# Performance work log

Hardware: AMD Instinct MI355X
Metric: run time of the kernel (lower is better)

## Reference

```python
import jax, jax.numpy as jnp
import numpy as np

C = 256
K = C // 2  # inter_channels


def setup_inputs() -> dict:
    key = jax.random.key(0)
    ks = jax.random.split(key, 9)
    B, H, W = 8, 64, 64
    x = jax.random.normal(ks[0], (B, C, H, W), dtype=jnp.float32)
    def lin(k, out_c, in_c, scale):
        return jax.random.normal(k, (out_c, in_c), dtype=jnp.float32) * scale
    s_in = 1.0 / np.sqrt(C)
    s_k = 1.0 / np.sqrt(K)
    return {
        "x": x,
        "theta_w": lin(ks[1], K, C, s_in), "theta_b": jnp.zeros((K,), jnp.float32),
        "phi_w":   lin(ks[2], K, C, s_in), "phi_b":   jnp.zeros((K,), jnp.float32),
        "g_w":     lin(ks[3], K, C, s_in), "g_b":     jnp.zeros((K,), jnp.float32),
        "out_w":   lin(ks[4], C, K, s_k),  "out_b":   jnp.zeros((C,), jnp.float32),
    }


def reference(x, theta_w, theta_b, phi_w, phi_b, g_w, g_b, out_w, out_b):
    B, Cc, H, W = x.shape
    N = H * W
    xf = x.reshape(B, Cc, N)  # [B, C, N]
    # 1x1 convs == per-pixel linear projections
    theta = jnp.einsum('bcn,kc->bnk', xf, theta_w) + theta_b            # [B, N, K]
    phi   = jnp.einsum('bcn,kc->bkn', xf, phi_w) + phi_b[:, None]       # [B, K, N]
    g     = jnp.einsum('bcn,kc->bnk', xf, g_w) + g_b                    # [B, N, K]
    attn = jax.nn.softmax(jnp.einsum('bnk,bkm->bnm', theta, phi), axis=-1)  # [B, N, N]
    y = jnp.einsum('bnm,bmk->bnk', attn, g)                             # [B, N, K]
    out = jnp.einsum('bnk,ck->bcn', y, out_w) + out_b[:, None]          # [B, C, N]
    return out.reshape(B, Cc, H, W) + x
```

## Files before the change

kernel.cpp:

```cpp
#include <hip/hip_runtime.h>

typedef __attribute__((ext_vector_type(8))) _Float16 f16x8;
typedef __attribute__((ext_vector_type(2))) _Float16 f16x2;
typedef __attribute__((ext_vector_type(4))) float f32x4;
typedef __attribute__((ext_vector_type(16))) float f32x16;
typedef __attribute__((ext_vector_type(2))) int int2v;
typedef __attribute__((ext_vector_type(4))) int int4v;

#define DEVI __device__ __forceinline__

DEVI unsigned short f2h(float f){
  _Float16 h = (_Float16)f;
  return __builtin_bit_cast(unsigned short, h);
}
DEVI float fexp2(float x){ return __builtin_amdgcn_exp2f(x); }

__global__ __launch_bounds__(256) void k_wconv(
    const float* __restrict__ tw, const float* __restrict__ pw,
    const float* __restrict__ gw, const float* __restrict__ ow,
    unsigned short* __restrict__ dst){
  int i = blockIdx.x*256 + threadIdx.x;
  int a = i>>15, off = i & 32767;
  const float* s = (a==0)?tw:(a==1)?pw:(a==2)?gw:ow;
  dst[i] = f2h(s[off]);
}

__global__ __launch_bounds__(256) void k_proj(
    const float* __restrict__ x,
    const unsigned short* __restrict__ Wq, const unsigned short* __restrict__ Wk,
    const unsigned short* __restrict__ Wg,
    const float* __restrict__ tb, const float* __restrict__ pb,
    const float* __restrict__ gb,
    unsigned short* __restrict__ Q, unsigned short* __restrict__ Km,
    unsigned short* __restrict__ VT)
{
  __shared__ __align__(16) unsigned short xT[64*264];
  const int tid = threadIdx.x;
  const int w = tid>>6, l = tid&63, l15 = l&15, lhi = l>>4;
  const int b = blockIdx.y, n0 = blockIdx.x*64;

  const float* xb = x + (size_t)b*256*4096 + n0;
  #pragma unroll 4
  for (int i=0;i<32;++i){
    int c = 64*w + 2*i;
    float v0 = xb[(size_t)c*4096 + l];
    float v1 = xb[(size_t)(c+1)*4096 + l];
    unsigned int pk = (unsigned int)f2h(v0) | ((unsigned int)f2h(v1)<<16);
    *(unsigned int*)&xT[l*264 + c] = pk;
  }
  __syncthreads();

  for (int mat=0; mat<2; ++mat){
    const unsigned short* Wm = mat ? Wk : Wq;
    const float* bias = mat ? pb : tb;
    unsigned short* Out = mat ? Km : Q;
    const float scl = mat ? 1.0f : 1.44269504f;
    for (int pbk=0; pbk<4; ++pbk){
      f16x8 aF[8];
      #pragma unroll
      for (int ks=0;ks<8;++ks)
        aF[ks] = *(const f16x8*)&xT[(16*pbk + l15)*264 + lhi*8 + 32*ks];
      #pragma unroll
      for (int kb2=0; kb2<2; ++kb2){
        int kb = 2*w + kb2;
        f32x4 acc = {0.f,0.f,0.f,0.f};
        #pragma unroll
        for (int ks=0;ks<8;++ks){
          f16x8 bF = *(const f16x8*)&Wm[(size_t)(16*kb + l15)*256 + lhi*8 + 32*ks];
          acc = __builtin_amdgcn_mfma_f32_16x16x32_f16(aF[ks], bF, acc, 0,0,0);
        }
        float bv = bias[16*kb + l15];
        #pragma unroll
        for (int r=0;r<4;++r){
          int pix = 16*pbk + lhi*4 + r;
          Out[((size_t)b*4096 + n0 + pix)*128 + 16*kb + l15] = f2h((acc[r] + bv)*scl);
        }
      }
    }
  }

  for (int nb=0; nb<4; ++nb){
    f16x8 bF[8];
    #pragma unroll
    for (int ks=0;ks<8;++ks)
      bF[ks] = *(const f16x8*)&xT[(16*nb + l15)*264 + lhi*8 + 32*ks];
    #pragma unroll
    for (int mb2=0; mb2<2; ++mb2){
      int mb = 2*w + mb2;
      f32x4 acc = {0.f,0.f,0.f,0.f};
      #pragma unroll
      for (int ks=0;ks<8;++ks){
        f16x8 aF = *(const f16x8*)&Wg[(size_t)(16*mb + l15)*256 + lhi*8 + 32*ks];
        acc = __builtin_amdgcn_mfma_f32_16x16x32_f16(aF, bF[ks], acc, 0,0,0);
      }
      #pragma unroll
      for (int r=0;r<4;++r){
        int k = 16*mb + lhi*4 + r;
        VT[((size_t)b*128 + k)*4096 + n0 + 16*nb + l15] = f2h(acc[r] + gb[k]);
      }
    }
  }
}

DEVI void stage_tiles(const char* Kg, const char* Vg, int nt,
                      char* Kd, char* Vd, int w, int l){
  #pragma unroll
  for (int c=0;c<4;++c){
    int base = (4*w + c)*1024;
    int lin  = base + l*16;
    int row = lin>>8, colb = lin&255;
    int f = ((row&7) ^ ((row>>2)&4)) << 4;
    const char* g = Kg + (size_t)(nt*64 + row)*256 + (colb ^ f);
    __builtin_amdgcn_global_load_lds((const __attribute__((address_space(1))) void*)g,
        (__attribute__((address_space(3))) void*)(Kd + base), 16, 0, 0);
  }
  #pragma unroll
  for (int c=0;c<4;++c){
    int base = (4*w + c)*1024;
    int lin  = base + l*16;
    int row = lin>>7, colb = lin&127;
    int f = ((row&7) ^ ((row>>2)&4)) << 4;
    const char* g = Vg + (size_t)row*8192 + (size_t)nt*128 + (colb ^ f);
    __builtin_amdgcn_global_load_lds((const __attribute__((address_space(1))) void*)g,
        (__attribute__((address_space(3))) void*)(Vd + base), 16, 0, 0);
  }
}

__global__ __launch_bounds__(256, 2) void k_attn(
    const unsigned short* __restrict__ Q, const unsigned short* __restrict__ Km,
    const unsigned short* __restrict__ VT,
    unsigned short* __restrict__ On,
    float* __restrict__ Mp, float* __restrict__ Lp)
{
  __shared__ __align__(16) unsigned short K_lds[2][64*128];
  __shared__ __align__(16) unsigned short V_lds[2][128*64];
  const int tid = threadIdx.x;
  const int w = tid>>6, l = tid&63;
  const int q32 = l & 31, hi = l >> 5;
  const int qt = blockIdx.x, h = blockIdx.y, b = blockIdx.z;
  const int n0 = qt*128, wq0 = w*32, nt0 = h*32;
  const int swz = ((q32&7) ^ ((q32>>2)&4)) << 4;

  const unsigned short* Qrow = Q + ((size_t)b*4096 + n0 + wq0 + q32)*128;
  f16x8 qf[8];
  #pragma unroll
  for (int ks=0; ks<8; ++ks)
    qf[ks] = *(const f16x8*)&Qrow[ks*16 + hi*8];

  const char* Kg = (const char*)(Km + (size_t)b*4096*128);
  const char* Vg = (const char*)(VT + (size_t)b*128*4096);

  float m_run = -3.0e38f, l_run = 0.f;
  f32x16 ob[4] = {};

  stage_tiles(Kg, Vg, nt0, (char*)K_lds[0], (char*)V_lds[0], w, l);
  __syncthreads();

  for (int it=0; it<32; ++it){
    const int cur = it & 1;
    if (it+1 < 32)
      stage_tiles(Kg, Vg, nt0+it+1, (char*)K_lds[cur^1], (char*)V_lds[cur^1], w, l);

    const char* Kc = (const char*)K_lds[cur];
    f32x16 st[2];
    #pragma unroll
    for (int mt=0; mt<2; ++mt){
      f32x16 a = {};
      int rb = (32*mt + q32)*256;
      #pragma unroll
      for (int ks=0; ks<8; ++ks){
        f16x8 kf = *(const f16x8*)(Kc + rb + ((16*hi + 32*ks) ^ swz));
        a = __builtin_amdgcn_mfma_f32_32x32x16_f16(kf, qf[ks], a, 0,0,0);
      }
      st[mt] = a;
    }

    float mx = -3.0e38f;
    #pragma unroll
    for (int mt=0; mt<2; ++mt)
      #pragma unroll
      for (int r=0; r<16; r+=4){
        float m01 = fmaxf(st[mt][r], st[mt][r+1]);
        mx = fmaxf(mx, fmaxf(m01, fmaxf(st[mt][r+2], st[mt][r+3])));
      }
    mx = fmaxf(mx, __shfl_xor(mx, 32));
    if (!__all(mx <= m_run + 11.5416f)){
      float mn = fmaxf(m_run, mx);
      float sc = fexp2(m_run - mn);
      l_run *= sc;
      #pragma unroll
      for (int db=0; db<4; ++db) ob[db] *= sc;
      m_run = mn;
    }
    float ps = 0.f;
    #pragma unroll
    for (int mt=0; mt<2; ++mt)
      #pragma unroll
      for (int r=0; r<16; ++r){
        float p = fexp2(st[mt][r] - m_run);
        st[mt][r] = p; ps += p;
      }
    l_run += ps + __shfl_xor(ps, 32);

    const char* Vc = (const char*)V_lds[cur];
    #pragma unroll
    for (int ks=0; ks<4; ++ks){
      const int mt = ks>>1, u = ks&1;
      int X0 = __builtin_bit_cast(int, __builtin_amdgcn_cvt_pkrtz(st[mt][8*u+0], st[mt][8*u+1]));
      int X1 = __builtin_bit_cast(int, __builtin_amdgcn_cvt_pkrtz(st[mt][8*u+2], st[mt][8*u+3]));
      int Y0 = __builtin_bit_cast(int, __builtin_amdgcn_cvt_pkrtz(st[mt][8*u+4], st[mt][8*u+5]));
      int Y1 = __builtin_bit_cast(int, __builtin_amdgcn_cvt_pkrtz(st[mt][8*u+6], st[mt][8*u+7]));
      int2v rA = __builtin_amdgcn_permlane32_swap(X0, Y0, false, false);
      int2v rB = __builtin_amdgcn_permlane32_swap(X1, Y1, false, false);
      int4v wv = {rA[0], rB[0], rA[1], rB[1]};
      f16x8 pf = __builtin_bit_cast(f16x8, wv);
      #pragma unroll
      for (int db=0; db<4; ++db){
        f16x8 vf = *(const f16x8*)(Vc + (32*db + q32)*128 + ((16*hi + 32*ks) ^ swz));
        ob[db] = __builtin_amdgcn_mfma_f32_32x32x16_f16(vf, pf, ob[db], 0,0,0);
      }
    }
    __syncthreads();
  }

  float invl = 1.0f / l_run;
  unsigned short* Orow = On + (((size_t)(h*8 + b)*4096) + n0 + wq0 + q32)*128;
  #pragma unroll
  for (int db=0; db<4; ++db)
    #pragma unroll
    for (int g=0; g<4; ++g){
      int2v pk2;
      pk2[0] = __builtin_bit_cast(int, __builtin_amdgcn_cvt_pkrtz(ob[db][4*g+0]*invl, ob[db][4*g+1]*invl));
      pk2[1] = __builtin_bit_cast(int, __builtin_amdgcn_cvt_pkrtz(ob[db][4*g+2]*invl, ob[db][4*g+3]*invl));
      *(int2v*)&Orow[32*db + 8*g + 4*hi] = pk2;
    }
  if (l < 32){
    size_t idx = (size_t)(h*8+b)*4096 + n0 + wq0 + l;
    Mp[idx] = m_run;
    Lp[idx] = l_run;
  }
}

__global__ __launch_bounds__(256) void k_merge(
    const unsigned short* __restrict__ On, const float* __restrict__ Mp,
    const float* __restrict__ Lp,
    const unsigned short* __restrict__ Wo, const float* __restrict__ out_b,
    const float* __restrict__ x, float* __restrict__ out)
{
  __shared__ __align__(16) unsigned short y_lds[32*136];
  const int tid = threadIdx.x;
  const int b = blockIdx.y, n0 = blockIdx.x*32;

  {
    int row = tid>>3, dq = (tid&7)*16;
    size_t i0 = (size_t)b*4096 + n0 + row;
    size_t i1 = (size_t)(8+b)*4096 + n0 + row;
    float m0 = Mp[i0], m1 = Mp[i1], l0 = Lp[i0], l1 = Lp[i1];
    float M = fmaxf(m0, m1);
    float a0 = fexp2(m0 - M)*l0, a1 = fexp2(m1 - M)*l1;
    float inv = 1.0f/(a0 + a1);
    float w0 = a0*inv, w1 = a1*inv;
    const unsigned short* p0 = On + i0*128 + dq;
    const unsigned short* p1 = On + i1*128 + dq;
    #pragma unroll
    for (int i=0;i<2;++i){
      f16x8 o0 = *(const f16x8*)&p0[8*i];
      f16x8 o1 = *(const f16x8*)&p1[8*i];
      int4v pk;
      #pragma unroll
      for (int j=0;j<4;++j){
        float ya = w0*(float)o0[2*j]   + w1*(float)o1[2*j];
        float yb = w0*(float)o0[2*j+1] + w1*(float)o1[2*j+1];
        pk[j] = __builtin_bit_cast(int, __builtin_amdgcn_cvt_pkrtz(ya, yb));
      }
      *(int4v*)&y_lds[row*136 + dq + 8*i] = pk;
    }
  }
  __syncthreads();

  const int w = tid>>6, l = tid&63, l15 = l&15, lhi = l>>4;
  const float* xb = x + (size_t)b*256*4096;
  const f32x4 zero4 = {0.f,0.f,0.f,0.f};
  for (int cb=0; cb<4; ++cb){
    int c0 = 64*w + 16*cb;
    f16x8 aW[4];
    #pragma unroll
    for (int ks=0;ks<4;++ks)
      aW[ks] = *(const f16x8*)&Wo[(size_t)(c0 + l15)*128 + lhi*8 + 32*ks];
    float obv[4];
    #pragma unroll
    for (int r=0;r<4;++r) obv[r] = out_b[c0 + lhi*4 + r];
    #pragma unroll
    for (int nb=0;nb<2;++nb){
      f32x4 acc = zero4;
      #pragma unroll
      for (int ks=0;ks<4;++ks){
        f16x8 yF = *(const f16x8*)&y_lds[(16*nb + l15)*136 + lhi*8 + 32*ks];
        acc = __builtin_amdgcn_mfma_f32_16x16x32_f16(aW[ks], yF, acc, 0,0,0);
      }
      #pragma unroll
      for (int r=0;r<4;++r){
        int c = c0 + lhi*4 + r;
        size_t oi = (size_t)c*4096 + n0 + 16*nb + l15;
        out[(size_t)b*256*4096 + oi] = acc[r] + obv[r] + xb[oi];
      }
    }
  }
}

extern "C" void kernel_launch(void* const* d_in, const int* in_sizes, int n_in,
                              void* d_out, int out_size, void* d_ws, size_t ws_size,
                              hipStream_t stream) {
  (void)in_sizes; (void)n_in; (void)out_size; (void)ws_size;
  const float* x  = (const float*)d_in[0];
  const float* tw = (const float*)d_in[1];
  const float* tb = (const float*)d_in[2];
  const float* pw = (const float*)d_in[3];
  const float* pb = (const float*)d_in[4];
  const float* gw = (const float*)d_in[5];
  const float* gb = (const float*)d_in[6];
  const float* ow = (const float*)d_in[7];
  const float* ob = (const float*)d_in[8];
  float* out = (float*)d_out;

  unsigned short* ws = (unsigned short*)d_ws;
  unsigned short* Wq = ws;
  unsigned short* Wk = ws + 32768;
  unsigned short* Wg = ws + 65536;
  unsigned short* Wo = ws + 98304;
  unsigned short* Q  = ws + 131072;
  unsigned short* Km = Q  + 4194304;
  unsigned short* VT = Km + 4194304;
  unsigned short* On = VT + 4194304;
  float* Mp = (float*)(On + 8388608);
  float* Lp = Mp + 65536;

  hipLaunchKernelGGL(k_wconv, dim3(512), dim3(256), 0, stream, tw, pw, gw, ow, ws);
  hipLaunchKernelGGL(k_proj,  dim3(64,8), dim3(256), 0, stream,
                     x, Wq, Wk, Wg, tb, pb, gb, Q, Km, VT);
  hipLaunchKernelGGL(k_attn,  dim3(32,2,8), dim3(256), 0, stream,
                     Q, Km, VT, On, Mp, Lp);
  hipLaunchKernelGGL(k_merge, dim3(128,8), dim3(256), 0, stream,
                     On, Mp, Lp, Wo, ob, x, out);
}
```

Baseline: 132.1 us.

## Halve KV tile, raise attention occupancy, and generalize split-KV merge

The attention kernel now stages 32-key K/V tiles instead of 64, with new LDS swizzles, and declares 4 blocks per CU instead of 2. The KV sequence is split 4 ways when the workspace is large enough, otherwise 2 ways. The merge kernel is templated on the split count so it can combine any number of partial outputs. The aim is more resident waves and more blocks to hide latency in the attention loop. The cost is more barriers per unit of work and extra partial-output traffic for the merge step to read.

```diff
diff --git a/kernel.cpp b/kernel.cpp
--- a/kernel.cpp
+++ b/kernel.cpp
@@ -1,7 +1,6 @@
 #include <hip/hip_runtime.h>
 
 typedef __attribute__((ext_vector_type(8))) _Float16 f16x8;
-typedef __attribute__((ext_vector_type(2))) _Float16 f16x2;
 typedef __attribute__((ext_vector_type(4))) float f32x4;
 typedef __attribute__((ext_vector_type(16))) float f32x16;
 typedef __attribute__((ext_vector_type(2))) int int2v;
@@ -105,41 +104,43 @@
 DEVI void stage_tiles(const char* Kg, const char* Vg, int nt,
                       char* Kd, char* Vd, int w, int l){
   #pragma unroll
-  for (int c=0;c<4;++c){
-    int base = (4*w + c)*1024;
+  for (int c=0;c<2;++c){
+    int base = (2*w + c)*1024;
     int lin  = base + l*16;
     int row = lin>>8, colb = lin&255;
-    int f = ((row&7) ^ ((row>>2)&4)) << 4;
-    const char* g = Kg + (size_t)(nt*64 + row)*256 + (colb ^ f);
+    int f = (row&7)<<4;
+    const char* g = Kg + (size_t)(nt*32 + row)*256 + (colb ^ f);
     __builtin_amdgcn_global_load_lds((const __attribute__((address_space(1))) void*)g,
         (__attribute__((address_space(3))) void*)(Kd + base), 16, 0, 0);
   }
   #pragma unroll
-  for (int c=0;c<4;++c){
-    int base = (4*w + c)*1024;
+  for (int c=0;c<2;++c){
+    int base = (2*w + c)*1024;
     int lin  = base + l*16;
-    int row = lin>>7, colb = lin&127;
-    int f = ((row&7) ^ ((row>>2)&4)) << 4;
-    const char* g = Vg + (size_t)row*8192 + (size_t)nt*128 + (colb ^ f);
+    int row = lin>>6, colb = lin&63;
+    int f = ((row>>1)&3)<<4;
+    const char* g = Vg + (size_t)row*8192 + (size_t)nt*64 + (colb ^ f);
     __builtin_amdgcn_global_load_lds((const __attribute__((address_space(1))) void*)g,
         (__attribute__((address_space(3))) void*)(Vd + base), 16, 0, 0);
   }
 }
 
-__global__ __launch_bounds__(256, 2) void k_attn(
+__global__ __launch_bounds__(256, 4) void k_attn(
     const unsigned short* __restrict__ Q, const unsigned short* __restrict__ Km,
     const unsigned short* __restrict__ VT,
     unsigned short* __restrict__ On,
-    float* __restrict__ Mp, float* __restrict__ Lp)
+    float* __restrict__ Mp, float* __restrict__ Lp,
+    int IT)
 {
-  __shared__ __align__(16) unsigned short K_lds[2][64*128];
-  __shared__ __align__(16) unsigned short V_lds[2][128*64];
+  __shared__ __align__(16) unsigned short K_lds[2][32*128];
+  __shared__ __align__(16) unsigned short V_lds[2][128*32];
   const int tid = threadIdx.x;
   const int w = tid>>6, l = tid&63;
   const int q32 = l & 31, hi = l >> 5;
   const int qt = blockIdx.x, h = blockIdx.y, b = blockIdx.z;
-  const int n0 = qt*128, wq0 = w*32, nt0 = h*32;
-  const int swz = ((q32&7) ^ ((q32>>2)&4)) << 4;
+  const int n0 = qt*128, wq0 = w*32, nt0 = h*IT;
+  const int swzK = (q32&7)<<4;
+  const int swzV = ((q32>>1)&3)<<4;
 
   const unsigned short* Qrow = Q + ((size_t)b*4096 + n0 + wq0 + q32)*128;
   f16x8 qf[8];
@@ -156,33 +157,28 @@
   stage_tiles(Kg, Vg, nt0, (char*)K_lds[0], (char*)V_lds[0], w, l);
   __syncthreads();
 
-  for (int it=0; it<32; ++it){
+  for (int it=0; it<IT; ++it){
     const int cur = it & 1;
-    if (it+1 < 32)
+    if (it+1 < IT)
       stage_tiles(Kg, Vg, nt0+it+1, (char*)K_lds[cur^1], (char*)V_lds[cur^1], w, l);
 
     const char* Kc = (const char*)K_lds[cur];
-    f32x16 st[2];
-    #pragma unroll
-    for (int mt=0; mt<2; ++mt){
-      f32x16 a = {};
-      int rb = (32*mt + q32)*256;
+    f32x16 st = {};
+    {
+      int rb = q32*256;
       #pragma unroll
       for (int ks=0; ks<8; ++ks){
-        f16x8 kf = *(const f16x8*)(Kc + rb + ((16*hi + 32*ks) ^ swz));
-        a = __builtin_amdgcn_mfma_f32_32x32x16_f16(kf, qf[ks], a, 0,0,0);
-      }
-      st[mt] = a;
+        f16x8 kf = *(const f16x8*)(Kc + rb + ((16*hi + 32*ks) ^ swzK));
+        st = __builtin_amdgcn_mfma_f32_32x32x16_f16(kf, qf[ks], st, 0,0,0);
+      }
     }
 
     float mx = -3.0e38f;
     #pragma unroll
-    for (int mt=0; mt<2; ++mt)
-      #pragma unroll
-      for (int r=0; r<16; r+=4){
-        float m01 = fmaxf(st[mt][r], st[mt][r+1]);
-        mx = fmaxf(mx, fmaxf(m01, fmaxf(st[mt][r+2], st[mt][r+3])));
-      }
+    for (int r=0; r<16; r+=4){
+      float m01 = fmaxf(st[r], st[r+1]);
+      mx = fmaxf(mx, fmaxf(m01, fmaxf(st[r+2], st[r+3])));
+    }
     mx = fmaxf(mx, __shfl_xor(mx, 32));
     if (!__all(mx <= m_run + 11.5416f)){
       float mn = fmaxf(m_run, mx);
@@ -194,29 +190,26 @@
     }
     float ps = 0.f;
     #pragma unroll
-    for (int mt=0; mt<2; ++mt)
-      #pragma unroll
-      for (int r=0; r<16; ++r){
-        float p = fexp2(st[mt][r] - m_run);
-        st[mt][r] = p; ps += p;
-      }
+    for (int r=0; r<16; ++r){
+      float p = fexp2(st[r] - m_run);
+      st[r] = p; ps += p;
+    }
     l_run += ps + __shfl_xor(ps, 32);
 
     const char* Vc = (const char*)V_lds[cur];
     #pragma unroll
-    for (int ks=0; ks<4; ++ks){
-      const int mt = ks>>1, u = ks&1;
-      int X0 = __builtin_bit_cast(int, __builtin_amdgcn_cvt_pkrtz(st[mt][8*u+0], st[mt][8*u+1]));
-      int X1 = __builtin_bit_cast(int, __builtin_amdgcn_cvt_pkrtz(st[mt][8*u+2], st[mt][8*u+3]));
-      int Y0 = __builtin_bit_cast(int, __builtin_amdgcn_cvt_pkrtz(st[mt][8*u+4], st[mt][8*u+5]));
-      int Y1 = __builtin_bit_cast(int, __builtin_amdgcn_cvt_pkrtz(st[mt][8*u+6], st[mt][8*u+7]));
+    for (int ks=0; ks<2; ++ks){
+      int X0 = __builtin_bit_cast(int, __builtin_amdgcn_cvt_pkrtz(st[8*ks+0], st[8*ks+1]));
+      int X1 = __builtin_bit_cast(int, __builtin_amdgcn_cvt_pkrtz(st[8*ks+2], st[8*ks+3]));
+      int Y0 = __builtin_bit_cast(int, __builtin_amdgcn_cvt_pkrtz(st[8*ks+4], st[8*ks+5]));
+      int Y1 = __builtin_bit_cast(int, __builtin_amdgcn_cvt_pkrtz(st[8*ks+6], st[8*ks+7]));
       int2v rA = __builtin_amdgcn_permlane32_swap(X0, Y0, false, false);
       int2v rB = __builtin_amdgcn_permlane32_swap(X1, Y1, false, false);
       int4v wv = {rA[0], rB[0], rA[1], rB[1]};
       f16x8 pf = __builtin_bit_cast(f16x8, wv);
       #pragma unroll
       for (int db=0; db<4; ++db){
-        f16x8 vf = *(const f16x8*)(Vc + (32*db + q32)*128 + ((16*hi + 32*ks) ^ swz));
+        f16x8 vf = *(const f16x8*)(Vc + (32*db + q32)*64 + ((16*hi + 32*ks) ^ swzV));
         ob[db] = __builtin_amdgcn_mfma_f32_32x32x16_f16(vf, pf, ob[db], 0,0,0);
       }
     }
@@ -241,6 +234,7 @@
   }
 }
 
+template<int S>
 __global__ __launch_bounds__(256) void k_merge(
     const unsigned short* __restrict__ On, const float* __restrict__ Mp,
     const float* __restrict__ Lp,
@@ -253,26 +247,34 @@
 
   {
     int row = tid>>3, dq = (tid&7)*16;
-    size_t i0 = (size_t)b*4096 + n0 + row;
-    size_t i1 = (size_t)(8+b)*4096 + n0 + row;
-    float m0 = Mp[i0], m1 = Mp[i1], l0 = Lp[i0], l1 = Lp[i1];
-    float M = fmaxf(m0, m1);
-    float a0 = fexp2(m0 - M)*l0, a1 = fexp2(m1 - M)*l1;
-    float inv = 1.0f/(a0 + a1);
-    float w0 = a0*inv, w1 = a1*inv;
-    const unsigned short* p0 = On + i0*128 + dq;
-    const unsigned short* p1 = On + i1*128 + dq;
+    float m[S], lv[S];
+    #pragma unroll
+    for (int s=0;s<S;++s){
+      size_t idx = (size_t)(s*8+b)*4096 + n0 + row;
+      m[s] = Mp[idx]; lv[s] = Lp[idx];
+    }
+    float M = m[0];
+    #pragma unroll
+    for (int s=1;s<S;++s) M = fmaxf(M, m[s]);
+    float wgt[S]; float wsum = 0.f;
+    #pragma unroll
+    for (int s=0;s<S;++s){ wgt[s] = fexp2(m[s]-M)*lv[s]; wsum += wgt[s]; }
+    float inv = 1.0f/wsum;
+    #pragma unroll
+    for (int s=0;s<S;++s) wgt[s] *= inv;
     #pragma unroll
     for (int i=0;i<2;++i){
-      f16x8 o0 = *(const f16x8*)&p0[8*i];
-      f16x8 o1 = *(const f16x8*)&p1[8*i];
+      float acc[8] = {};
+      #pragma unroll
+      for (int s=0;s<S;++s){
+        f16x8 o = *(const f16x8*)&On[((size_t)(s*8+b)*4096 + n0 + row)*128 + dq + 8*i];
+        #pragma unroll
+        for (int j=0;j<8;++j) acc[j] += wgt[s]*(float)o[j];
+      }
       int4v pk;
       #pragma unroll
-      for (int j=0;j<4;++j){
-        float ya = w0*(float)o0[2*j]   + w1*(float)o1[2*j];
-        float yb = w0*(float)o0[2*j+1] + w1*(float)o1[2*j+1];
-        pk[j] = __builtin_bit_cast(int, __builtin_amdgcn_cvt_pkrtz(ya, yb));
-      }
+      for (int j=0;j<4;++j)
+        pk[j] = __builtin_bit_cast(int, __builtin_amdgcn_cvt_pkrtz(acc[2*j], acc[2*j+1]));
       *(int4v*)&y_lds[row*136 + dq + 8*i] = pk;
     }
   }
@@ -311,7 +313,7 @@
 extern "C" void kernel_launch(void* const* d_in, const int* in_sizes, int n_in,
                               void* d_out, int out_size, void* d_ws, size_t ws_size,
                               hipStream_t stream) {
-  (void)in_sizes; (void)n_in; (void)out_size; (void)ws_size;
+  (void)in_sizes; (void)n_in; (void)out_size;
   const float* x  = (const float*)d_in[0];
   const float* tw = (const float*)d_in[1];
   const float* tb = (const float*)d_in[2];
@@ -323,6 +325,9 @@
   const float* ob = (const float*)d_in[8];
   float* out = (float*)d_out;
 
+  const int S = (ws_size >= 60030976ull) ? 4 : 2;
+  const int IT = 128 / S;
+
   unsigned short* ws = (unsigned short*)d_ws;
   unsigned short* Wq = ws;
   unsigned short* Wk = ws + 32768;
@@ -332,14 +337,18 @@
   unsigned short* Km = Q  + 4194304;
   unsigned short* VT = Km + 4194304;
   unsigned short* On = VT + 4194304;
-  float* Mp = (float*)(On + 8388608);
-  float* Lp = Mp + 65536;
+  float* Mp = (float*)(On + (size_t)S*4194304);
+  float* Lp = Mp + (size_t)S*32768;
 
   hipLaunchKernelGGL(k_wconv, dim3(512), dim3(256), 0, stream, tw, pw, gw, ow, ws);
   hipLaunchKernelGGL(k_proj,  dim3(64,8), dim3(256), 0, stream,
                      x, Wq, Wk, Wg, tb, pb, gb, Q, Km, VT);
-  hipLaunchKernelGGL(k_attn,  dim3(32,2,8), dim3(256), 0, stream,
-                     Q, Km, VT, On, Mp, Lp);
-  hipLaunchKernelGGL(k_merge, dim3(128,8), dim3(256), 0, stream,
-                     On, Mp, Lp, Wo, ob, x, out);
-}
+  hipLaunchKernelGGL(k_attn,  dim3(32,S,8), dim3(256), 0, stream,
+                     Q, Km, VT, On, Mp, Lp, IT);
+  if (S == 4)
+    hipLaunchKernelGGL(k_merge<4>, dim3(128,8), dim3(256), 0, stream,
+                       On, Mp, Lp, Wo, ob, x, out);
+  else
+    hipLaunchKernelGGL(k_merge<2>, dim3(128,8), dim3(256), 0, stream,
+                       On, Mp, Lp, Wo, ob, x, out);
+}
```

Result: slower. 184.2 us (+39.4%).
